# Optimization experiments

Measured on AMD Instinct MI355X. Metric: run time of the kernel, lower is better.

## Reference

```python
import jax, jax.numpy as jnp
import numpy as np

B, N, DIM = 2, 2048, 1024
H, DH = 16, 64
INNER = H * DH
SCALE = DH ** -0.5


def rotate_half(x):
    x1, x2 = jnp.split(x, 2, axis=-1)
    return jnp.concatenate((-x2, x1), axis=-1)


def apply_rotary(pos, t):
    # pos: [n, dh] broadcast against t: [b, h, n, dh]
    return t * jnp.cos(pos) + rotate_half(t) * jnp.sin(pos)


def setup_inputs() -> dict:
    key = jax.random.key(0)
    ks = jax.random.split(key, 5)
    x = jax.random.normal(ks[0], (B, N, DIM), dtype=jnp.float32)
    rotary_emb = jax.random.normal(ks[1], (N, DH), dtype=jnp.float32)
    w_qkv = jax.random.normal(ks[2], (3 * INNER, DIM), dtype=jnp.float32) * (DIM ** -0.5)
    w_out = jax.random.normal(ks[3], (DIM, INNER), dtype=jnp.float32) * (INNER ** -0.5)
    b_out = jax.random.normal(ks[4], (DIM,), dtype=jnp.float32) * 0.01
    return {"x": x, "rotary_emb": rotary_emb, "w_qkv": w_qkv, "w_out": w_out, "b_out": b_out}


def reference(x, rotary_emb, w_qkv, w_out, b_out):
    b, n, _ = x.shape
    qkv = jnp.einsum('bnd,ed->bne', x, w_qkv)  # [b, n, 3*inner]
    q, k, v = jnp.split(qkv, 3, axis=-1)
    # [b, n, inner] -> [b, h, n, dh]
    reshape = lambda t: t.reshape(b, n, H, DH).transpose(0, 2, 1, 3)
    q, k, v = reshape(q), reshape(k), reshape(v)
    q = apply_rotary(rotary_emb, q)
    k = apply_rotary(rotary_emb, k)
    dots = jnp.einsum('bhid,bhjd->bhij', q, k) * SCALE
    attn = jax.nn.softmax(dots, axis=-1)
    out = jnp.einsum('bhij,bhjd->bhid', attn, v)
    out = out.transpose(0, 2, 1, 3).reshape(b, n, INNER)
    return jnp.einsum('bne,de->bnd', out, w_out) + b_out
```

## Files before the change

kernel.cpp:

```cpp
#include <hip/hip_runtime.h>
#include <math.h>

typedef unsigned short ushort_t;
typedef __attribute__((ext_vector_type(8))) short short8v;
typedef __attribute__((ext_vector_type(4))) float float4v;

#define BB 2
#define NN 2048
#define HH 16
#define DHH 64
#define DIMM 1024
#define QKV3 3072
#define INNERR 1024
#define QSCALE 0.1803368801111244f

__device__ __forceinline__ ushort_t f2bf(float f) {
    unsigned u = __float_as_uint(f);
    u += 0x7fffu + ((u >> 16) & 1u);
    return (ushort_t)(u >> 16);
}
__device__ __forceinline__ float bf2f(unsigned h) {
    return __uint_as_float(h << 16);
}
__device__ __forceinline__ unsigned pk_bf16(float a, float b) {
#if __has_builtin(__builtin_amdgcn_cvt_pk_bf16_f32)
    typedef __attribute__((ext_vector_type(2))) __bf16 bf16x2;
    bf16x2 r = __builtin_amdgcn_cvt_pk_bf16_f32(a, b);
    return __builtin_bit_cast(unsigned, r);
#else
    return (unsigned)f2bf(a) | ((unsigned)f2bf(b) << 16);
#endif
}
__device__ __forceinline__ float fast_exp2(float x) {
#if __has_builtin(__builtin_amdgcn_exp2f)
    return __builtin_amdgcn_exp2f(x);
#else
    return exp2f(x);
#endif
}
__device__ __forceinline__ void gl2lds16(const void* g, void* l) {
    __builtin_amdgcn_global_load_lds(
        (const __attribute__((address_space(1))) unsigned int*)g,
        (__attribute__((address_space(3))) unsigned int*)l, 16, 0, 0);
}

__global__ __launch_bounds__(256) void conv_fused(const float* __restrict__ x,
                                                  const float* __restrict__ wqkv,
                                                  const float* __restrict__ wout,
                                                  ushort_t* __restrict__ xo,
                                                  ushort_t* __restrict__ wqkvo,
                                                  ushort_t* __restrict__ wouto) {
    int blk = blockIdx.x;
    const float* in; ushort_t* out; int i;
    if (blk < 4096)      { in = x;    out = xo;    i = blk * 256 + threadIdx.x; }
    else if (blk < 7168) { in = wqkv; out = wqkvo; i = (blk - 4096) * 256 + threadIdx.x; }
    else                 { in = wout; out = wouto; i = (blk - 7168) * 256 + threadIdx.x; }
    float4 v = ((const float4*)in)[i];
    ushort4 o;
    o.x = f2bf(v.x); o.y = f2bf(v.y); o.z = f2bf(v.z); o.w = f2bf(v.w);
    ((ushort4*)out)[i] = o;
}

template <int NOUT, bool BF16OUT, bool BIAS, bool ROT>
__global__ __launch_bounds__(256, 3) void gemm128(const ushort_t* __restrict__ A,
                                                  const ushort_t* __restrict__ Bm,
                                                  const float* __restrict__ bias,
                                                  const float* __restrict__ rot,
                                                  ushort_t* __restrict__ Vt,
                                                  void* __restrict__ Cout, int K) {
    constexpr int NCH = 4;
    __shared__ ushort_t As[2][128 * 32];
    __shared__ ushort_t Bs[2][128 * 32];
    const int t = threadIdx.x;
    const int lane = t & 63;
    const int w = t >> 6;
    const int wr = w >> 1;
    const int wc = w & 1;
    const int quad = lane >> 4;
    const int l15 = lane & 15;
    const int m0 = blockIdx.y * 128;
    const int n0 = blockIdx.x * 128;

    float4v acc[4][4];
#pragma unroll
    for (int i = 0; i < 4; ++i)
#pragma unroll
        for (int j = 0; j < 4; ++j) acc[i][j] = (float4v)0.0f;

    int srow[NCH], slc[NCH], sdst[NCH];
    bool sisA[NCH];
#pragma unroll
    for (int u = 0; u < NCH; ++u) {
        int c = u * 256 + t;
        if (c < 512) {
            int row = c >> 2;
            sisA[u] = true; srow[u] = row; slc[u] = (c & 3) ^ ((row >> 1) & 3); sdst[u] = c * 8;
        } else {
            int cb = c - 512;
            int row = cb >> 2;
            sisA[u] = false; srow[u] = row; slc[u] = (cb & 3) ^ ((row >> 1) & 3); sdst[u] = cb * 8;
        }
    }
#pragma unroll
    for (int u = 0; u < NCH; ++u) {
        if (sisA[u]) gl2lds16(&A[(size_t)(m0 + srow[u]) * K + slc[u] * 8], &As[0][sdst[u]]);
        else         gl2lds16(&Bm[(size_t)(n0 + srow[u]) * K + slc[u] * 8], &Bs[0][sdst[u]]);
    }
    const int NIT = K >> 5;
    for (int it = 0; it < NIT; ++it) {
        const int cur = it & 1;
        if (it + 1 < NIT) {
            const int nxt = cur ^ 1;
            const int kc = (it + 1) << 5;
#pragma unroll
            for (int u = 0; u < NCH; ++u) {
                if (sisA[u]) gl2lds16(&A[(size_t)(m0 + srow[u]) * K + kc + slc[u] * 8], &As[nxt][sdst[u]]);
                else         gl2lds16(&Bm[(size_t)(n0 + srow[u]) * K + kc + slc[u] * 8], &Bs[nxt][sdst[u]]);
            }
            asm volatile("s_waitcnt vmcnt(4)\n\ts_barrier" ::: "memory");
        } else {
            asm volatile("s_waitcnt vmcnt(0)\n\ts_barrier" ::: "memory");
        }
        short8v a[4], b[4];
#pragma unroll
        for (int i = 0; i < 4; ++i) {
            int row = wr * 64 + i * 16 + l15;
            int pc = quad ^ ((row >> 1) & 3);
            a[i] = *(const short8v*)&As[cur][row * 32 + pc * 8];
        }
#pragma unroll
        for (int j = 0; j < 4; ++j) {
            int row = wc * 64 + j * 16 + l15;
            int pc = quad ^ ((row >> 1) & 3);
            b[j] = *(const short8v*)&Bs[cur][row * 32 + pc * 8];
        }
#pragma unroll
        for (int i = 0; i < 4; ++i)
#pragma unroll
            for (int j = 0; j < 4; ++j)
                acc[i][j] = __builtin_amdgcn_mfma_f32_16x16x32_bf16(a[i], b[j], acc[i][j], 0, 0, 0);
        asm volatile("s_barrier" ::: "memory");
    }
    const int region = ROT ? (n0 >> 10) : 0;
    if (ROT && region == 2) {
#pragma unroll
        for (int i = 0; i < 4; ++i) {
            int grow = m0 + wr * 64 + i * 16 + quad * 4;
            int bb = grow >> 11, nn_ = grow & (NN - 1);
            int tk = nn_ & 63;
            int tp = (tk & 32) | ((tk & 12) << 1) | ((tk & 16) >> 2);
            int nstore = (nn_ & ~63) | tp;
#pragma unroll
            for (int j = 0; j < 4; ++j) {
                int vcol = n0 + wc * 64 + j * 16 + l15 - 2048;
                int hh = vcol >> 6, dh = vcol & 63;
                uint2 st;
                st.x = pk_bf16(acc[i][j][0], acc[i][j][1]);
                st.y = pk_bf16(acc[i][j][2], acc[i][j][3]);
                *(uint2*)&Vt[((size_t)(bb * HH + hh) * DHH + dh) * NN + nstore] = st;
            }
        }
        return;
    }
    if (ROT) {
        float scale = (region == 0) ? QSCALE : 1.0f;
#pragma unroll
        for (int i = 0; i < 4; ++i) {
#pragma unroll
            for (int r = 0; r < 4; ++r) {
                int n = (m0 + wr * 64 + i * 16 + quad * 4 + r) & (NN - 1);
#pragma unroll
                for (int jl = 0; jl < 2; ++jl) {
                    int dh = jl * 16 + l15;
                    float plo = rot[n * DHH + dh];
                    float phi = rot[n * DHH + dh + 32];
                    float lo = acc[i][jl][r], hi = acc[i][jl + 2][r];
                    acc[i][jl][r]     = (lo * __cosf(plo) - hi * __sinf(plo)) * scale;
                    acc[i][jl + 2][r] = (hi * __cosf(phi) + lo * __sinf(phi)) * scale;
                }
            }
        }
    }
#pragma unroll
    for (int i = 0; i < 4; ++i) {
        int grow = m0 + wr * 64 + i * 16 + quad * 4;
#pragma unroll
        for (int j = 0; j < 4; ++j) {
            int gcol = n0 + wc * 64 + j * 16 + l15;
            float bv = BIAS ? bias[gcol] : 0.0f;
#pragma unroll
            for (int r = 0; r < 4; ++r) {
                float v = acc[i][j][r] + bv;
                if (BF16OUT)
                    ((ushort_t*)Cout)[(size_t)(grow + r) * NOUT + gcol] = f2bf(v);
                else
                    ((float*)Cout)[(size_t)(grow + r) * NOUT + gcol] = v;
            }
        }
    }
}

template <int NOUT, bool BF16OUT, bool BIAS, bool ROT>
__global__ __launch_bounds__(256, 6) void gemm_bf16(const ushort_t* __restrict__ A,
                                                    const ushort_t* __restrict__ Bm,
                                                    const float* __restrict__ bias,
                                                    const float* __restrict__ rot,
                                                    ushort_t* __restrict__ Vt,
                                                    void* __restrict__ Cout, int K) {
    constexpr int NCH = 3;
    __shared__ ushort_t As[2][128 * 32];
    __shared__ ushort_t Bs[2][64 * 32];
    const int t = threadIdx.x;
    const int lane = t & 63;
    const int w = t >> 6;
    const int quad = lane >> 4;
    const int l15 = lane & 15;
    const int m0 = blockIdx.y * 128;
    const int n0 = blockIdx.x * 64;
    const int wm = w * 32;

    float4v acc[2][4];
#pragma unroll
    for (int i = 0; i < 2; ++i)
#pragma unroll
        for (int j = 0; j < 4; ++j) acc[i][j] = (float4v)0.0f;

    int srow[NCH], slc[NCH], sdst[NCH];
    bool sisA[NCH];
#pragma unroll
    for (int u = 0; u < NCH; ++u) {
        int c = u * 256 + t;
        if (c < 512) {
            int row = c >> 2;
            sisA[u] = true; srow[u] = row; slc[u] = (c & 3) ^ ((row >> 1) & 3); sdst[u] = c * 8;
        } else {
            int cb = c - 512;
            int row = cb >> 2;
            sisA[u] = false; srow[u] = row; slc[u] = (cb & 3) ^ ((row >> 1) & 3); sdst[u] = cb * 8;
        }
    }
#pragma unroll
    for (int u = 0; u < NCH; ++u) {
        if (sisA[u]) gl2lds16(&A[(size_t)(m0 + srow[u]) * K + slc[u] * 8], &As[0][sdst[u]]);
        else         gl2lds16(&Bm[(size_t)(n0 + srow[u]) * K + slc[u] * 8], &Bs[0][sdst[u]]);
    }
    const int NIT = K >> 5;
    for (int it = 0; it < NIT; ++it) {
        const int cur = it & 1;
        if (it + 1 < NIT) {
            const int nxt = cur ^ 1;
            const int kc = (it + 1) << 5;
#pragma unroll
            for (int u = 0; u < NCH; ++u) {
                if (sisA[u]) gl2lds16(&A[(size_t)(m0 + srow[u]) * K + kc + slc[u] * 8], &As[nxt][sdst[u]]);
                else         gl2lds16(&Bm[(size_t)(n0 + srow[u]) * K + kc + slc[u] * 8], &Bs[nxt][sdst[u]]);
            }
            asm volatile("s_waitcnt vmcnt(3)\n\ts_barrier" ::: "memory");
        } else {
            asm volatile("s_waitcnt vmcnt(0)\n\ts_barrier" ::: "memory");
        }
        short8v a[2], b[4];
#pragma unroll
        for (int i = 0; i < 2; ++i) {
            int row = wm + i * 16 + l15;
            int pc = quad ^ ((row >> 1) & 3);
            a[i] = *(const short8v*)&As[cur][row * 32 + pc * 8];
        }
#pragma unroll
        for (int j = 0; j < 4; ++j) {
            int row = j * 16 + l15;
            int pc = quad ^ ((row >> 1) & 3);
            b[j] = *(const short8v*)&Bs[cur][row * 32 + pc * 8];
        }
#pragma unroll
        for (int i = 0; i < 2; ++i)
#pragma unroll
            for (int j = 0; j < 4; ++j)
                acc[i][j] = __builtin_amdgcn_mfma_f32_16x16x32_bf16(a[i], b[j], acc[i][j], 0, 0, 0);
        asm volatile("s_barrier" ::: "memory");
    }
#pragma unroll
    for (int i = 0; i < 2; ++i) {
        int grow = m0 + wm + i * 16 + quad * 4;
#pragma unroll
        for (int j = 0; j < 4; ++j) {
            int gcol = n0 + j * 16 + l15;
            float bv = BIAS ? bias[gcol] : 0.0f;
#pragma unroll
            for (int r = 0; r < 4; ++r) {
                float v = acc[i][j][r] + bv;
                if (BF16OUT)
                    ((ushort_t*)Cout)[(size_t)(grow + r) * NOUT + gcol] = f2bf(v);
                else
                    ((float*)Cout)[(size_t)(grow + r) * NOUT + gcol] = v;
            }
        }
    }
}

__global__ __launch_bounds__(256, 4) void flash_mfma(const ushort_t* __restrict__ qkv,
                                                     const ushort_t* __restrict__ Vt,
                                                     ushort_t* __restrict__ po,
                                                     float* __restrict__ lp) {
    __shared__ ushort_t smem[16384];
    ushort_t* Osc = smem;
    const int t = threadIdx.x;
    const int lane = t & 63;
    const int w = t >> 6;
    const int quad = lane >> 4;
    const int l15 = lane & 15;
    const int blk = blockIdx.x;
    const int slot = blk >> 3;
    const int ks = slot & 1;
    const int qt = (slot >> 1) & 15;
    const int bh = (blk & 7) * 4 + (slot >> 5);
    const int b = bh >> 4, h = bh & 15;
    const int n0 = qt * 128;

    short8v bq[2][2];
#pragma unroll
    for (int g = 0; g < 2; ++g) {
        size_t qb = (size_t)(b * NN + n0 + w * 32 + g * 16 + l15) * QKV3 + h * DHH + quad * 8;
        bq[g][0] = *(const short8v*)&qkv[qb];
        bq[g][1] = *(const short8v*)&qkv[qb + 32];
    }
    float4v o_acc[2][4];
    float4v l_acc[2];
#pragma unroll
    for (int g = 0; g < 2; ++g) {
        l_acc[g] = (float4v)0.0f;
#pragma unroll
        for (int nb = 0; nb < 4; ++nb) o_acc[g][nb] = (float4v)0.0f;
    }
    const short one_bf = (short)0x3F80;
    short8v ones8 = {one_bf, one_bf, one_bf, one_bf, one_bf, one_bf, one_bf, one_bf};

    const int s0 = t, s1 = 256 + t;
    const int r0 = s0 >> 3, lc0 = (s0 & 7) ^ (r0 & 7);
    const int r1 = s1 >> 3, lc1 = (s1 & 7) ^ (r1 & 7);
    const int koff0 = r0 * QKV3 + lc0 * 8, koff1 = r1 * QKV3 + lc1 * 8;
    const int voff0 = r0 * NN + lc0 * 8,   voff1 = r1 * NN + lc1 * 8;
    const ushort_t* kp = qkv + (size_t)b * NN * QKV3 + INNERR + h * DHH + (size_t)ks * 1024 * QKV3;
    const ushort_t* vp = Vt + (size_t)(b * HH + h) * DHH * NN + ks * 1024;

    {
        gl2lds16(kp + koff0, smem + 0 * 4096 + s0 * 8);
        gl2lds16(kp + koff1, smem + 0 * 4096 + s1 * 8);
        gl2lds16(vp + voff0, smem + 2 * 4096 + s0 * 8);
        gl2lds16(vp + voff1, smem + 2 * 4096 + s1 * 8);
    }
    for (int jt = 0; jt < 16; ++jt) {
        const int cur = jt & 1;
        if (jt < 15) {
            kp += 64 * QKV3;
            vp += 64;
            const int nxt = cur ^ 1;
            gl2lds16(kp + koff0, smem + nxt * 4096 + s0 * 8);
            gl2lds16(kp + koff1, smem + nxt * 4096 + s1 * 8);
            gl2lds16(vp + voff0, smem + (2 + nxt) * 4096 + s0 * 8);
            gl2lds16(vp + voff1, smem + (2 + nxt) * 4096 + s1 * 8);
            asm volatile("s_waitcnt vmcnt(4)\n\ts_barrier" ::: "memory");
        } else {
            asm volatile("s_waitcnt vmcnt(0)\n\ts_barrier" ::: "memory");
        }
        const ushort_t* Ksc = smem + cur * 4096;
        const ushort_t* Vtc = smem + (2 + cur) * 4096;
        float4v s_acc[2][4];
#pragma unroll
        for (int g = 0; g < 2; ++g)
#pragma unroll
            for (int nb = 0; nb < 4; ++nb) s_acc[g][nb] = (float4v)0.0f;
#pragma unroll
        for (int kb = 0; kb < 2; ++kb)
#pragma unroll
            for (int nb = 0; nb < 4; ++nb) {
                int row = nb * 16 + l15;
                int pc = (kb * 4 + quad) ^ (row & 7);
                short8v ak = *(const short8v*)&Ksc[row * 64 + pc * 8];
                s_acc[0][nb] = __builtin_amdgcn_mfma_f32_16x16x32_bf16(ak, bq[0][kb], s_acc[0][nb], 0, 0, 0);
                s_acc[1][nb] = __builtin_amdgcn_mfma_f32_16x16x32_bf16(ak, bq[1][kb], s_acc[1][nb], 0, 0, 0);
            }
#pragma unroll
        for (int g = 0; g < 2; ++g) {
            float p[4][4];
#pragma unroll
            for (int nb = 0; nb < 4; ++nb)
#pragma unroll
                for (int r = 0; r < 4; ++r) p[nb][r] = fast_exp2(s_acc[g][nb][r]);
            uint4 u0, u1;
            u0.x = pk_bf16(p[0][0], p[0][1]); u0.y = pk_bf16(p[0][2], p[0][3]);
            u0.z = pk_bf16(p[1][0], p[1][1]); u0.w = pk_bf16(p[1][2], p[1][3]);
            u1.x = pk_bf16(p[2][0], p[2][1]); u1.y = pk_bf16(p[2][2], p[2][3]);
            u1.z = pk_bf16(p[3][0], p[3][1]); u1.w = pk_bf16(p[3][2], p[3][3]);
            short8v ap0 = __builtin_bit_cast(short8v, u0);
            short8v ap1 = __builtin_bit_cast(short8v, u1);
            l_acc[g] = __builtin_amdgcn_mfma_f32_16x16x32_bf16(ap0, ones8, l_acc[g], 0, 0, 0);
            l_acc[g] = __builtin_amdgcn_mfma_f32_16x16x32_bf16(ap1, ones8, l_acc[g], 0, 0, 0);
#pragma unroll
            for (int nb = 0; nb < 4; ++nb) {
                int row = nb * 16 + l15;
                int pc0 = quad ^ (row & 7);
                int pc1 = (4 + quad) ^ (row & 7);
                short8v bv0 = *(const short8v*)&Vtc[row * 64 + pc0 * 8];
                short8v bv1 = *(const short8v*)&Vtc[row * 64 + pc1 * 8];
                o_acc[g][nb] = __builtin_amdgcn_mfma_f32_16x16x32_bf16(ap0, bv0, o_acc[g][nb], 0, 0, 0);
                o_acc[g][nb] = __builtin_amdgcn_mfma_f32_16x16x32_bf16(ap1, bv1, o_acc[g][nb], 0, 0, 0);
            }
        }
        asm volatile("s_barrier" ::: "memory");
    }
#pragma unroll
    for (int g = 0; g < 2; ++g) {
        if (l15 == 0)
            *(float4*)&lp[(size_t)(ks * 32 + bh) * NN + n0 + w * 32 + g * 16 + quad * 4] =
                *(float4*)&l_acc[g];
    }
    ushort_t* osc = Osc + w * (32 * 68);
#pragma unroll
    for (int g = 0; g < 2; ++g)
#pragma unroll
        for (int nb = 0; nb < 4; ++nb)
#pragma unroll
            for (int r = 0; r < 4; ++r)
                osc[(g * 16 + quad * 4 + r) * 68 + nb * 16 + l15] = f2bf(o_acc[g][nb][r]);
    __builtin_amdgcn_s_waitcnt(0);
    {
        int rr = lane >> 1, c0 = (lane & 1) * 32;
        size_t prow = ((size_t)(ks * 32 + bh) * NN + n0 + w * 32 + rr) * DHH + c0;
#pragma unroll
        for (int u = 0; u < 4; ++u) {
            uint4 v = *(const uint4*)&osc[rr * 68 + c0 + u * 8];
            *(uint4*)&po[prow + u * 8] = v;
        }
    }
}

__global__ __launch_bounds__(256) void reduce_o(const ushort_t* __restrict__ po,
                                                const float* __restrict__ lp,
                                                ushort_t* __restrict__ attn) {
    int tg = blockIdx.x * 256 + threadIdx.x;
    int bh = tg >> 15;
    int rem = tg & 32767;
    int n = rem >> 4;
    int dh0 = (rem & 15) * 4;
    size_t p0 = ((size_t)bh * NN + n) * DHH + dh0;
    size_t p1 = p0 + (size_t)32 * NN * DHH;
    uint2 a = *(const uint2*)&po[p0];
    uint2 c = *(const uint2*)&po[p1];
    float inv = 1.0f / (lp[(size_t)bh * NN + n] + lp[(size_t)(32 + bh) * NN + n]);
    float o0 = (bf2f(a.x & 0xffff) + bf2f(c.x & 0xffff)) * inv;
    float o1 = (bf2f(a.x >> 16)    + bf2f(c.x >> 16))    * inv;
    float o2 = (bf2f(a.y & 0xffff) + bf2f(c.y & 0xffff)) * inv;
    float o3 = (bf2f(a.y >> 16)    + bf2f(c.y >> 16))    * inv;
    int b = bh >> 4, h = bh & 15;
    uint2 st;
    st.x = pk_bf16(o0, o1);
    st.y = pk_bf16(o2, o3);
    *(uint2*)&attn[((size_t)(b * NN + n)) * INNERR + h * DHH + dh0] = st;
}

extern "C" void kernel_launch(void* const* d_in, const int* in_sizes, int n_in,
                              void* d_out, int out_size, void* d_ws, size_t ws_size,
                              hipStream_t stream) {
    const float* x = (const float*)d_in[0];
    const float* rot = (const float*)d_in[1];
    const float* w_qkv = (const float*)d_in[2];
    const float* w_out = (const float*)d_in[3];
    const float* b_out = (const float*)d_in[4];
    float* y = (float*)d_out;

    char* ws = (char*)d_ws;
    ushort_t* qkv_bf  = (ushort_t*)(ws);
    ushort_t* vt_bf   = (ushort_t*)(ws + 25165824);
    ushort_t* wout_bf = (ushort_t*)(ws + 33554432);
    ushort_t* wqkv_bf = (ushort_t*)(ws + 35651584);
    float*    lp      = (float*)(ws + 35651584);
    ushort_t* x_bf    = (ushort_t*)(ws + 41943040);
    ushort_t* attn_bf = x_bf;
    ushort_t* po      = (ushort_t*)(ws + 50331648);

    conv_fused<<<8192, 256, 0, stream>>>(x, w_qkv, w_out, x_bf, wqkv_bf, wout_bf);
    gemm128<QKV3, true, false, true><<<dim3(24, 32), 256, 0, stream>>>(
        x_bf, wqkv_bf, nullptr, rot, vt_bf, qkv_bf, DIMM);
    flash_mfma<<<1024, 256, 0, stream>>>(qkv_bf, vt_bf, po, lp);
    reduce_o<<<4096, 256, 0, stream>>>(po, lp, attn_bf);
    gemm_bf16<INNERR, false, true, false><<<dim3(16, 32), 256, 0, stream>>>(
        attn_bf, wout_bf, b_out, nullptr, nullptr, y, INNERR);
}
```

Baseline: 188.5 us.

## Double flash attention query tile per block and hoist K/V fragment loads

Each flash block now handles 256 query rows (64 per wave) instead of 128, halving the grid to 512 blocks. K and V fragments for each 64-key tile are loaded from LDS once into registers and reused across four query groups, which cuts LDS reads per MFMA and the per-query cost of streaming K/V. The output staging is split into two passes so it still fits the shared buffer. Register pressure roughly doubles for the accumulators (launch bound relaxed to 2 blocks), which lowers occupancy. With only 512 blocks the grid may fill the GPU less evenly.

```diff
diff --git a/kernel.cpp b/kernel.cpp
--- a/kernel.cpp
+++ b/kernel.cpp
@@ -298,12 +298,11 @@
     }
 }
 
-__global__ __launch_bounds__(256, 4) void flash_mfma(const ushort_t* __restrict__ qkv,
+__global__ __launch_bounds__(256, 2) void flash_mfma(const ushort_t* __restrict__ qkv,
                                                      const ushort_t* __restrict__ Vt,
                                                      ushort_t* __restrict__ po,
                                                      float* __restrict__ lp) {
     __shared__ ushort_t smem[16384];
-    ushort_t* Osc = smem;
     const int t = threadIdx.x;
     const int lane = t & 63;
     const int w = t >> 6;
@@ -312,28 +311,29 @@
     const int blk = blockIdx.x;
     const int slot = blk >> 3;
     const int ks = slot & 1;
-    const int qt = (slot >> 1) & 15;
-    const int bh = (blk & 7) * 4 + (slot >> 5);
+    const int qt = (slot >> 1) & 7;
+    const int bh = (blk & 7) * 4 + (slot >> 4);
     const int b = bh >> 4, h = bh & 15;
-    const int n0 = qt * 128;
-
-    short8v bq[2][2];
-#pragma unroll
-    for (int g = 0; g < 2; ++g) {
-        size_t qb = (size_t)(b * NN + n0 + w * 32 + g * 16 + l15) * QKV3 + h * DHH + quad * 8;
+    const int n0 = qt * 256;
+
+    short8v bq[4][2];
+#pragma unroll
+    for (int g = 0; g < 4; ++g) {
+        size_t qb = (size_t)(b * NN + n0 + w * 64 + g * 16 + l15) * QKV3 + h * DHH + quad * 8;
         bq[g][0] = *(const short8v*)&qkv[qb];
         bq[g][1] = *(const short8v*)&qkv[qb + 32];
     }
-    float4v o_acc[2][4];
-    float4v l_acc[2];
-#pragma unroll
-    for (int g = 0; g < 2; ++g) {
+    float4v o_acc[4][4];
+    float4v l_acc[4];
+#pragma unroll
+    for (int g = 0; g < 4; ++g) {
         l_acc[g] = (float4v)0.0f;
 #pragma unroll
         for (int nb = 0; nb < 4; ++nb) o_acc[g][nb] = (float4v)0.0f;
     }
     const short one_bf = (short)0x3F80;
     short8v ones8 = {one_bf, one_bf, one_bf, one_bf, one_bf, one_bf, one_bf, one_bf};
+    const float4v ZR = (float4v)0.0f;
 
     const int s0 = t, s1 = 256 + t;
     const int r0 = s0 >> 3, lc0 = (s0 & 7) ^ (r0 & 7);
@@ -365,28 +365,31 @@
         }
         const ushort_t* Ksc = smem + cur * 4096;
         const ushort_t* Vtc = smem + (2 + cur) * 4096;
-        float4v s_acc[2][4];
-#pragma unroll
-        for (int g = 0; g < 2; ++g)
-#pragma unroll
-            for (int nb = 0; nb < 4; ++nb) s_acc[g][nb] = (float4v)0.0f;
-#pragma unroll
-        for (int kb = 0; kb < 2; ++kb)
-#pragma unroll
-            for (int nb = 0; nb < 4; ++nb) {
-                int row = nb * 16 + l15;
-                int pc = (kb * 4 + quad) ^ (row & 7);
-                short8v ak = *(const short8v*)&Ksc[row * 64 + pc * 8];
-                s_acc[0][nb] = __builtin_amdgcn_mfma_f32_16x16x32_bf16(ak, bq[0][kb], s_acc[0][nb], 0, 0, 0);
-                s_acc[1][nb] = __builtin_amdgcn_mfma_f32_16x16x32_bf16(ak, bq[1][kb], s_acc[1][nb], 0, 0, 0);
-            }
-#pragma unroll
-        for (int g = 0; g < 2; ++g) {
+        short8v ak[2][4], bv[2][4];
+#pragma unroll
+        for (int nb = 0; nb < 4; ++nb) {
+            int row = nb * 16 + l15;
+            int base = row * 64;
+            int r7 = row & 7;
+            ak[0][nb] = *(const short8v*)&Ksc[base + ((quad) ^ r7) * 8];
+            ak[1][nb] = *(const short8v*)&Ksc[base + ((4 + quad) ^ r7) * 8];
+            bv[0][nb] = *(const short8v*)&Vtc[base + ((quad) ^ r7) * 8];
+            bv[1][nb] = *(const short8v*)&Vtc[base + ((4 + quad) ^ r7) * 8];
+        }
+#pragma unroll
+        for (int g = 0; g < 4; ++g) {
+            float4v s[4];
+#pragma unroll
+            for (int nb = 0; nb < 4; ++nb)
+                s[nb] = __builtin_amdgcn_mfma_f32_16x16x32_bf16(ak[0][nb], bq[g][0], ZR, 0, 0, 0);
+#pragma unroll
+            for (int nb = 0; nb < 4; ++nb)
+                s[nb] = __builtin_amdgcn_mfma_f32_16x16x32_bf16(ak[1][nb], bq[g][1], s[nb], 0, 0, 0);
             float p[4][4];
 #pragma unroll
             for (int nb = 0; nb < 4; ++nb)
 #pragma unroll
-                for (int r = 0; r < 4; ++r) p[nb][r] = fast_exp2(s_acc[g][nb][r]);
+                for (int r = 0; r < 4; ++r) p[nb][r] = fast_exp2(s[nb][r]);
             uint4 u0, u1;
             u0.x = pk_bf16(p[0][0], p[0][1]); u0.y = pk_bf16(p[0][2], p[0][3]);
             u0.z = pk_bf16(p[1][0], p[1][1]); u0.w = pk_bf16(p[1][2], p[1][3]);
@@ -398,40 +401,41 @@
             l_acc[g] = __builtin_amdgcn_mfma_f32_16x16x32_bf16(ap1, ones8, l_acc[g], 0, 0, 0);
 #pragma unroll
             for (int nb = 0; nb < 4; ++nb) {
-                int row = nb * 16 + l15;
-                int pc0 = quad ^ (row & 7);
-                int pc1 = (4 + quad) ^ (row & 7);
-                short8v bv0 = *(const short8v*)&Vtc[row * 64 + pc0 * 8];
-                short8v bv1 = *(const short8v*)&Vtc[row * 64 + pc1 * 8];
-                o_acc[g][nb] = __builtin_amdgcn_mfma_f32_16x16x32_bf16(ap0, bv0, o_acc[g][nb], 0, 0, 0);
-                o_acc[g][nb] = __builtin_amdgcn_mfma_f32_16x16x32_bf16(ap1, bv1, o_acc[g][nb], 0, 0, 0);
+                o_acc[g][nb] = __builtin_amdgcn_mfma_f32_16x16x32_bf16(ap0, bv[0][nb], o_acc[g][nb], 0, 0, 0);
+                o_acc[g][nb] = __builtin_amdgcn_mfma_f32_16x16x32_bf16(ap1, bv[1][nb], o_acc[g][nb], 0, 0, 0);
             }
         }
         asm volatile("s_barrier" ::: "memory");
     }
 #pragma unroll
-    for (int g = 0; g < 2; ++g) {
+    for (int g = 0; g < 4; ++g) {
         if (l15 == 0)
-            *(float4*)&lp[(size_t)(ks * 32 + bh) * NN + n0 + w * 32 + g * 16 + quad * 4] =
+            *(float4*)&lp[(size_t)(ks * 32 + bh) * NN + n0 + w * 64 + g * 16 + quad * 4] =
                 *(float4*)&l_acc[g];
     }
-    ushort_t* osc = Osc + w * (32 * 68);
-#pragma unroll
-    for (int g = 0; g < 2; ++g)
-#pragma unroll
-        for (int nb = 0; nb < 4; ++nb)
-#pragma unroll
-            for (int r = 0; r < 4; ++r)
-                osc[(g * 16 + quad * 4 + r) * 68 + nb * 16 + l15] = f2bf(o_acc[g][nb][r]);
-    __builtin_amdgcn_s_waitcnt(0);
-    {
-        int rr = lane >> 1, c0 = (lane & 1) * 32;
-        size_t prow = ((size_t)(ks * 32 + bh) * NN + n0 + w * 32 + rr) * DHH + c0;
-#pragma unroll
-        for (int u = 0; u < 4; ++u) {
-            uint4 v = *(const uint4*)&osc[rr * 68 + c0 + u * 8];
-            *(uint4*)&po[prow + u * 8] = v;
-        }
+    ushort_t* osc = smem + w * (32 * 68);
+#pragma unroll
+    for (int pass = 0; pass < 2; ++pass) {
+#pragma unroll
+        for (int gg = 0; gg < 2; ++gg) {
+            int g = pass * 2 + gg;
+#pragma unroll
+            for (int nb = 0; nb < 4; ++nb)
+#pragma unroll
+                for (int r = 0; r < 4; ++r)
+                    osc[(gg * 16 + quad * 4 + r) * 68 + nb * 16 + l15] = f2bf(o_acc[g][nb][r]);
+        }
+        __builtin_amdgcn_s_waitcnt(0);
+        {
+            int rr = lane >> 1, c0 = (lane & 1) * 32;
+            size_t prow = ((size_t)(ks * 32 + bh) * NN + n0 + w * 64 + pass * 32 + rr) * DHH + c0;
+#pragma unroll
+            for (int u = 0; u < 4; ++u) {
+                uint4 v = *(const uint4*)&osc[rr * 68 + c0 + u * 8];
+                *(uint4*)&po[prow + u * 8] = v;
+            }
+        }
+        __builtin_amdgcn_s_waitcnt(0);
     }
 }
 
@@ -482,7 +486,7 @@
     conv_fused<<<8192, 256, 0, stream>>>(x, w_qkv, w_out, x_bf, wqkv_bf, wout_bf);
     gemm128<QKV3, true, false, true><<<dim3(24, 32), 256, 0, stream>>>(
         x_bf, wqkv_bf, nullptr, rot, vt_bf, qkv_bf, DIMM);
-    flash_mfma<<<1024, 256, 0, stream>>>(qkv_bf, vt_bf, po, lp);
+    flash_mfma<<<512, 256, 0, stream>>>(qkv_bf, vt_bf, po, lp);
     reduce_o<<<4096, 256, 0, stream>>>(po, lp, attn_bf);
     gemm_bf16<INNERR, false, true, false><<<dim3(16, 32), 256, 0, stream>>>(
         attn_bf, wout_bf, b_out, nullptr, nullptr, y, INNERR);
```

After: 188.8 us. About the same (+0.2%).
